# Optimization experiments

Hardware: AMD Instinct MI355X
Metric: run time of the kernel (lower is better)

Reference implementation:

```python
import jax, jax.numpy as jnp
import numpy as np

N = 262144
C = 81
NUM_HARD = 32768


def setup_inputs() -> dict:
    key = jax.random.key(0)
    k1, k2, k3, k4 = jax.random.split(key, 4)
    return {
        "cls_score": jax.random.normal(k1, (N, C), dtype=jnp.float32),
        "rois_label": jax.random.randint(k2, (N,), 0, C, dtype=jnp.int32),
        "bbox_pred": jax.random.normal(k3, (N, 4), dtype=jnp.float32),
        "rois_target": jax.random.normal(k4, (N, 4), dtype=jnp.float32),
        "rois_inside_ws": jnp.ones((N, 4), dtype=jnp.float32),
        "rois_outside_ws": jnp.ones((N, 4), dtype=jnp.float32),
        "num_hard": NUM_HARD,
    }


def reference(cls_score, rois_label, bbox_pred, rois_target,
              rois_inside_ws, rois_outside_ws, num_hard):
    num_classes = cls_score.shape[1]
    pos = rois_label > 0                                   # [N] bool
    num_pos = jnp.sum(pos.astype(jnp.float32))

    # --- hard-example mining on detached scores (no grad through selection) ---
    conf_p = jax.lax.stop_gradient(cls_score)              # [N, C]
    x_max = jnp.max(conf_p)                                # global scalar max (as in torch code)
    lse = jnp.log(jnp.sum(jnp.exp(conf_p - x_max), axis=1)) + x_max   # [N]
    gathered = jnp.take_along_axis(conf_p, rois_label[:, None].astype(jnp.int32), axis=1)[:, 0]
    loss_c = lse - gathered                                # [N]
    loss_c = jnp.where(pos, jnp.float32(100.0), loss_c)    # force positives in
    _, topk_idx = jax.lax.top_k(loss_c, num_hard)          # [num_hard]

    # --- weighted cross entropy on selected hard examples ---
    weight = jnp.ones((num_classes,), dtype=jnp.float32).at[0].set(num_pos / num_hard)
    sel_logits = cls_score[topk_idx]                       # [num_hard, C]
    sel_labels = rois_label[topk_idx]                      # [num_hard]
    logp = jax.nn.log_softmax(sel_logits, axis=1)
    nll = -jnp.take_along_axis(logp, sel_labels[:, None].astype(jnp.int32), axis=1)[:, 0]
    w = weight[sel_labels]
    loss_cls = jnp.sum(w * nll) / jnp.sum(w)               # torch weighted-mean CE

    # --- smooth L1 on positive rois only (masked; mean over num_pos*4 elems) ---
    diff = bbox_pred - rois_target                         # [N, 4]
    ad = jnp.abs(diff)
    sl1 = jnp.where(ad < 1.0, 0.5 * diff * diff, ad - 0.5)
    posf = pos.astype(sl1.dtype)[:, None]
    loss_box = jnp.sum(sl1 * posf) / (num_pos * 4.0)

    return loss_cls, loss_box
```

## Files before the change

kernel.cpp:

```cpp
#include <hip/hip_runtime.h>

#define NROWS 262144
#define NCLS  81
#define NTILES 4096
#define TILE_FLOATS 5184
#define KEY100 0xC2C80000u

__device__ __forceinline__ unsigned mono(float f) {
    unsigned u = __float_as_uint(f);
    return (u & 0x80000000u) ? ~u : (u | 0x80000000u);
}

__global__ __launch_bounds__(256) void row_kernel(
        const float* __restrict__ cls, const int* __restrict__ label,
        const float* __restrict__ bpred, const float* __restrict__ btgt,
        float4* __restrict__ partial)
{
    __shared__ float sm[TILE_FLOATS];
    __shared__ int slbl[64];
    __shared__ unsigned ru[3][4];
    __shared__ float rf[3][4];

    const int t = threadIdx.x;
    const int lane = t & 63, wid = t >> 6;
    const int blk = blockIdx.x;
    const int row = t >> 2, j = t & 3;

    int myLbl = label[blk*64 + row];
    if (t < 64) slbl[t] = label[blk*64 + t];
    float bsum = 0.f;
    {
        int gi = blk*256 + t;
        float p = bpred[gi], q = btgt[gi];
        if (myLbl > 0) {
            float d = p - q, ad = fabsf(d);
            bsum = (ad < 1.f) ? 0.5f*d*d : ad - 0.5f;
        }
    }

    {
        const float4* src = (const float4*)(cls + (size_t)blk * TILE_FLOATS);
        float4* dst = (float4*)sm;
        #pragma unroll
        for (int jj = 0; jj < 5; ++jj) dst[t + 256*jj] = src[t + 256*jj];
        if (t < 16) dst[t + 1280] = src[t + 1280];
    }
    __syncthreads();

    const float* rp = sm + row * NCLS;
    float s = 0.f;
    for (int i = j; i < NCLS; i += 4) s += __expf(rp[i]);
    s += __shfl_xor(s, 1);
    s += __shfl_xor(s, 2);

    unsigned pcnt = 0, gcnt = 0, ecnt = 0;
    float gtv = 0.f, pnv = 0.f;
    if (j == 0) {
        float lse = __logf(s);
        bool pos = myLbl > 0;
        float nll = lse - rp[myLbl];
        unsigned kk = mono(pos ? 100.0f : nll);
        pcnt = pos ? 1u : 0u;
        gcnt = (kk > KEY100) ? 1u : 0u;
        ecnt = (!pos && kk == KEY100) ? 1u : 0u;
        gtv  = (kk > KEY100) ? nll : 0.f;
        pnv  = pos ? nll : 0.f;
    }
    #pragma unroll
    for (int off = 32; off; off >>= 1) {
        pcnt += __shfl_xor(pcnt, off);
        gcnt += __shfl_xor(gcnt, off);
        ecnt += __shfl_xor(ecnt, off);
        gtv  += __shfl_xor(gtv, off);
        pnv  += __shfl_xor(pnv, off);
        bsum += __shfl_xor(bsum, off);
    }
    if (lane == 0) {
        ru[0][wid] = pcnt; ru[1][wid] = gcnt; ru[2][wid] = ecnt;
        rf[0][wid] = gtv;  rf[1][wid] = pnv;  rf[2][wid] = bsum;
    }
    __syncthreads();
    if (t == 0) {
        unsigned np = ru[0][0]+ru[0][1]+ru[0][2]+ru[0][3];
        unsigned ng = ru[1][0]+ru[1][1]+ru[1][2]+ru[1][3];
        unsigned ne = ru[2][0]+ru[2][1]+ru[2][2]+ru[2][3];
        float gt = rf[0][0]+rf[0][1]+rf[0][2]+rf[0][3];
        float pn = rf[1][0]+rf[1][1]+rf[1][2]+rf[1][3];
        float bx = rf[2][0]+rf[2][1]+rf[2][2]+rf[2][3];
        partial[blk] = make_float4(__uint_as_float(np | (ng<<8) | (ne<<16)), gt, pn, bx);
    }
}

__device__ void scan_desc_64k_1024(const unsigned* hist, unsigned k,
                                   unsigned* outB, unsigned* outRem,
                                   unsigned* wsum )
{
    const int t = threadIdx.x, lane = t & 63, wid = t >> 6;
    unsigned sum = 0;
    for (int j = 0; j < 64; ++j) sum += hist[65535 - (t*64 + j)];
    unsigned inc = sum;
    #pragma unroll
    for (int off = 1; off < 64; off <<= 1) {
        unsigned v = __shfl_up(inc, off);
        if (lane >= off) inc += v;
    }
    if (lane == 63) wsum[wid] = inc;
    __syncthreads();
    unsigned woff = 0;
    for (int w = 0; w < wid; ++w) woff += wsum[w];
    unsigned running = woff + inc - sum;
    for (int j = 0; j < 64; ++j) {
        unsigned bkt = 65535u - (unsigned)(t*64 + j);
        unsigned c = hist[bkt];
        if (running < k && running + c >= k) { *outB = bkt; *outRem = k - running; }
        running += c;
    }
}

__global__ __launch_bounds__(1024) void finalize_kernel(
        const float* __restrict__ cls, const int* __restrict__ label,
        const float4* __restrict__ partial, const int* __restrict__ d_num_hard,
        unsigned* __restrict__ hist, float* __restrict__ nllbuf,
        float* __restrict__ out)
{
    const int t = threadIdx.x, lane = t & 63, wid = t >> 6;
    __shared__ unsigned wNp[16], wNg[16], wNe[16];
    __shared__ float wPn[16], wGt[16], wBx[16];
    __shared__ unsigned sCross, sCumBefore;
    __shared__ float sFull, sPartial;
    __shared__ float sm[TILE_FLOATS];
    __shared__ float snll[64];
    __shared__ int slbl[64];

    unsigned npI[4]; float pnI[4];
    unsigned npS = 0, ngS = 0, neS = 0;
    float gtS = 0.f, pnS = 0.f, bxS = 0.f;
    #pragma unroll
    for (int i = 0; i < 4; ++i) {
        float4 v = partial[t*4 + i];
        unsigned c = __float_as_uint(v.x);
        npI[i] = c & 255u; pnI[i] = v.z;
        npS += npI[i]; ngS += (c >> 8) & 255u; neS += (c >> 16) & 255u;
        gtS += v.y; pnS += v.z; bxS += v.w;
    }
    unsigned incNp = npS; float incPn = pnS;
    #pragma unroll
    for (int off = 1; off < 64; off <<= 1) {
        unsigned v = __shfl_up(incNp, off);
        float    f = __shfl_up(incPn, off);
        if (lane >= off) { incNp += v; incPn += f; }
    }
    #pragma unroll
    for (int off = 32; off; off >>= 1) {
        ngS += __shfl_xor(ngS, off); neS += __shfl_xor(neS, off);
        gtS += __shfl_xor(gtS, off); bxS += __shfl_xor(bxS, off);
    }
    if (lane == 63) { wNp[wid] = incNp; wPn[wid] = incPn; }
    if (lane == 0)  { wNg[wid] = ngS; wNe[wid] = neS; wGt[wid] = gtS; wBx[wid] = bxS; }
    __syncthreads();

    unsigned NP = 0, NG = 0, NE = 0; float GT = 0.f, BX = 0.f;
    unsigned npOff = 0; float pnOff = 0.f;
    for (int w = 0; w < 16; ++w) {
        NP += wNp[w]; NG += wNg[w]; NE += wNe[w]; GT += wGt[w]; BX += wBx[w];
        if (w < wid) { npOff += wNp[w]; pnOff += wPn[w]; }
    }
    const unsigned k = (unsigned)(*d_num_hard);
    const bool fast = (NG < k) && (NG + NP >= k) && (NE == 0);

    if (fast) {
        const unsigned need = k - NG;
        unsigned cum = npOff + incNp - npS;
        float    fl  = pnOff + incPn - pnS;
        #pragma unroll
        for (int i = 0; i < 4; ++i) {
            if (cum < need && cum + npI[i] >= need) {
                sCross = (unsigned)(t*4 + i); sCumBefore = cum; sFull = fl;
            }
            cum += npI[i]; fl += pnI[i];
        }
        __syncthreads();

        {
            const float4* src = (const float4*)(cls + (size_t)sCross * TILE_FLOATS);
            float4* dst = (float4*)sm;
            dst[t] = src[t];
            if (t < 272) dst[t + 1024] = src[t + 1024];
            if (t < 64) slbl[t] = label[(int)sCross*64 + t];
        }
        __syncthreads();

        {
            const int brow = t >> 4, bj = t & 15;
            const float* rp = sm + brow * NCLS;
            float s = 0.f;
            for (int i = bj; i < NCLS; i += 16) s += __expf(rp[i]);
            s += __shfl_xor(s, 1);
            s += __shfl_xor(s, 2);
            s += __shfl_xor(s, 4);
            s += __shfl_xor(s, 8);
            if (bj == 0) snll[brow] = __logf(s) - rp[slbl[brow]];
        }
        __syncthreads();

        if (t < 64) {
            int lbl = slbl[t];
            bool pos = lbl > 0;
            unsigned long long m = __ballot(pos);
            unsigned rank = (unsigned)__popcll(m & ((1ull << t) - 1ull));
            unsigned rem = need - sCumBefore;
            float c = (pos && rank < rem) ? snll[t] : 0.f;
            #pragma unroll
            for (int off = 32; off; off >>= 1) c += __shfl_xor(c, off);
            if (t == 0) sPartial = c;
        }
        __syncthreads();
        if (t == 0) {
            float wgt0 = (float)NP / (float)k;
            out[0] = (wgt0*GT + sFull + sPartial) / (wgt0*NG + (float)need);
            out[1] = BX / ((float)NP * 4.0f);
        }
        return;
    }

    __shared__ unsigned wsum[16];
    __shared__ unsigned sB1, sKrem, sTkey, sNeed;
    __shared__ unsigned wEq[16];
    __shared__ float r1[16], r2[16];
    __syncthreads();

    for (int r = t; r < NROWS; r += 1024) {
        const float* rp = cls + (size_t)r * NCLS;
        float ssum = 0.f;
        for (int cix = 0; cix < NCLS; ++cix) ssum += __expf(rp[cix]);
        nllbuf[r] = __logf(ssum) - rp[label[r]];
    }
    __syncthreads();

    for (int i = t; i < 65536; i += 1024) hist[i] = 0u;
    __syncthreads();
    for (int base = 0; base < NROWS; base += 1024) {
        int r = base + t;
        unsigned key = mono(label[r] > 0 ? 100.0f : nllbuf[r]);
        unsigned bkt = key >> 16;
        unsigned long long active = __ballot(1);
        while (active) {
            int leader = (int)__builtin_ctzll(active);
            unsigned lb = __shfl(bkt, leader);
            unsigned long long grp = __ballot(bkt == lb) & active;
            if (lane == leader) atomicAdd(&hist[lb], (unsigned)__popcll(grp));
            active &= ~grp;
        }
    }
    __syncthreads();
    scan_desc_64k_1024(hist, k, &sB1, &sKrem, wsum);
    __syncthreads();

    for (int i = t; i < 65536; i += 1024) hist[i] = 0u;
    __syncthreads();
    for (int base = 0; base < NROWS; base += 1024) {
        int r = base + t;
        unsigned key = mono(label[r] > 0 ? 100.0f : nllbuf[r]);
        bool in = (key >> 16) == sB1;
        unsigned bkt = key & 0xFFFFu;
        unsigned long long active = __ballot(in);
        while (active) {
            int leader = (int)__builtin_ctzll(active);
            unsigned lb = __shfl(bkt, leader);
            unsigned long long grp = __ballot(in && bkt == lb) & active;
            if (lane == leader) atomicAdd(&hist[lb], (unsigned)__popcll(grp));
            active &= ~grp;
        }
    }
    __syncthreads();
    scan_desc_64k_1024(hist, sKrem, &sTkey, &sNeed, wsum);
    __syncthreads();
    if (t == 0) sTkey = (sB1 << 16) | sTkey;
    __syncthreads();

    const unsigned tkey = sTkey, need = sNeed;
    const float wgt0 = (float)NP / (float)k;
    float accN = 0.f, accW = 0.f;
    unsigned running = 0;
    for (int base = 0; base < NROWS; base += 1024) {
        int r = base + t;
        int lbl = label[r]; float v = nllbuf[r];
        unsigned key = mono(lbl > 0 ? 100.0f : v);
        bool eq = (key == tkey);
        unsigned long long b = __ballot(eq);
        if (lane == 0) wEq[wid] = (unsigned)__popcll(b);
        __syncthreads();
        unsigned woff = 0, chunkTotal = 0;
        for (int w = 0; w < 16; ++w) {
            chunkTotal += wEq[w];
            if (w < wid) woff += wEq[w];
        }
        unsigned rank = running + woff + (unsigned)__popcll(b & ((1ull << lane) - 1ull));
        bool sel = (key > tkey) || (eq && rank < need);
        if (sel) { float wg = (lbl == 0) ? wgt0 : 1.f; accN += wg * v; accW += wg; }
        running += chunkTotal;
        __syncthreads();
    }
    #pragma unroll
    for (int off = 32; off; off >>= 1) {
        accN += __shfl_xor(accN, off);
        accW += __shfl_xor(accW, off);
    }
    if (lane == 0) { r1[wid] = accN; r2[wid] = accW; }
    __syncthreads();
    if (t == 0) {
        float N = 0.f, W = 0.f;
        for (int w = 0; w < 16; ++w) { N += r1[w]; W += r2[w]; }
        out[0] = N / W;
        out[1] = BX / ((float)NP * 4.0f);
    }
}

extern "C" void kernel_launch(void* const* d_in, const int* in_sizes, int n_in,
                              void* d_out, int out_size, void* d_ws, size_t ws_size,
                              hipStream_t stream) {
    const float* cls   = (const float*)d_in[0];
    const int*   label = (const int*)d_in[1];
    const float* bpred = (const float*)d_in[2];
    const float* btgt  = (const float*)d_in[3];
    const int*   nh    = (const int*)d_in[6];
    float* out = (float*)d_out;

    char* ws = (char*)d_ws;
    float4*   partial = (float4*)(ws);
    unsigned* hist    = (unsigned*)(ws + 65536);
    float*    nllbuf  = (float*)(ws + 65536 + 262144);

    row_kernel<<<NTILES, 256, 0, stream>>>(cls, label, bpred, btgt, partial);
    finalize_kernel<<<1, 1024, 0, stream>>>(cls, label, partial, nh,
                                            hist, nllbuf, out);
}
```

Before: 29.15 us.

## Compute row exp-sums in registers with LDS atomics instead of staging tile

Stops staging the 64x81 logits tile in shared memory. Each thread now exponentiates its own coalesced float4 values in registers and accumulates per-row sums with shared-memory atomicAdd, splitting a float4 across rows where it straddles a row boundary. The per-row label logit is then read directly from global memory, and the count and partial-sum reductions are done by the first wave only. This is meant to cut LDS footprint, which could raise occupancy, and to remove a strided LDS read pass, at the cost of LDS atomic contention and an extra scattered global load per row.

```diff
diff --git a/kernel.cpp b/kernel.cpp
--- a/kernel.cpp
+++ b/kernel.cpp
@@ -16,18 +16,17 @@
         const float* __restrict__ bpred, const float* __restrict__ btgt,
         float4* __restrict__ partial)
 {
-    __shared__ float sm[TILE_FLOATS];
+    __shared__ float rowsum[64];
     __shared__ int slbl[64];
-    __shared__ unsigned ru[3][4];
-    __shared__ float rf[3][4];
+    __shared__ float wbs[4];
 
     const int t = threadIdx.x;
     const int lane = t & 63, wid = t >> 6;
     const int blk = blockIdx.x;
-    const int row = t >> 2, j = t & 3;
-
-    int myLbl = label[blk*64 + row];
-    if (t < 64) slbl[t] = label[blk*64 + t];
+
+    if (t < 64) { rowsum[t] = 0.f; slbl[t] = label[blk*64 + t]; }
+
+    int myLbl = label[blk*64 + (t >> 2)];
     float bsum = 0.f;
     {
         int gi = blk*256 + t;
@@ -38,56 +37,60 @@
         }
     }
 
-    {
-        const float4* src = (const float4*)(cls + (size_t)blk * TILE_FLOATS);
-        float4* dst = (float4*)sm;
+    const float4* src = (const float4*)(cls + (size_t)blk * TILE_FLOATS);
+    float4 v[6];
+    #pragma unroll
+    for (int jj = 0; jj < 6; ++jj)
+        if (jj < 5 || t < 16) v[jj] = src[t + 256*jj];
+
+    __syncthreads();
+
+    #pragma unroll
+    for (int jj = 0; jj < 6; ++jj) {
+        if (jj < 5 || t < 16) {
+            int le = (t + 256*jj) * 4;
+            int r0 = le / 81;
+            int c0 = le - r0*81;
+            float e0 = __expf(v[jj].x), e1 = __expf(v[jj].y);
+            float e2 = __expf(v[jj].z), e3 = __expf(v[jj].w);
+            if (c0 <= 77) {
+                atomicAdd(&rowsum[r0], (e0+e1)+(e2+e3));
+            } else {
+                int n0 = 81 - c0;
+                float a = e0 + (n0 > 1 ? e1 : 0.f) + (n0 > 2 ? e2 : 0.f);
+                float b = (n0 > 1 ? 0.f : e1) + (n0 > 2 ? 0.f : e2) + e3;
+                atomicAdd(&rowsum[r0], a);
+                atomicAdd(&rowsum[r0+1], b);
+            }
+        }
+    }
+    __syncthreads();
+
+    unsigned cnt = 0; float gtv = 0.f, pnv = 0.f;
+    if (t < 64) {
+        float lse = __logf(rowsum[t]);
+        int lbl = slbl[t];
+        bool pos = lbl > 0;
+        float nll = lse - cls[(size_t)(blk*64 + t)*NCLS + lbl];
+        unsigned kk = mono(pos ? 100.0f : nll);
+        cnt = (pos ? 1u : 0u) | ((kk > KEY100 ? 1u : 0u) << 8)
+            | (((!pos && kk == KEY100) ? 1u : 0u) << 16);
+        gtv = (kk > KEY100) ? nll : 0.f;
+        pnv = pos ? nll : 0.f;
         #pragma unroll
-        for (int jj = 0; jj < 5; ++jj) dst[t + 256*jj] = src[t + 256*jj];
-        if (t < 16) dst[t + 1280] = src[t + 1280];
-    }
-    __syncthreads();
-
-    const float* rp = sm + row * NCLS;
-    float s = 0.f;
-    for (int i = j; i < NCLS; i += 4) s += __expf(rp[i]);
-    s += __shfl_xor(s, 1);
-    s += __shfl_xor(s, 2);
-
-    unsigned pcnt = 0, gcnt = 0, ecnt = 0;
-    float gtv = 0.f, pnv = 0.f;
-    if (j == 0) {
-        float lse = __logf(s);
-        bool pos = myLbl > 0;
-        float nll = lse - rp[myLbl];
-        unsigned kk = mono(pos ? 100.0f : nll);
-        pcnt = pos ? 1u : 0u;
-        gcnt = (kk > KEY100) ? 1u : 0u;
-        ecnt = (!pos && kk == KEY100) ? 1u : 0u;
-        gtv  = (kk > KEY100) ? nll : 0.f;
-        pnv  = pos ? nll : 0.f;
-    }
-    #pragma unroll
-    for (int off = 32; off; off >>= 1) {
-        pcnt += __shfl_xor(pcnt, off);
-        gcnt += __shfl_xor(gcnt, off);
-        ecnt += __shfl_xor(ecnt, off);
-        gtv  += __shfl_xor(gtv, off);
-        pnv  += __shfl_xor(pnv, off);
-        bsum += __shfl_xor(bsum, off);
-    }
-    if (lane == 0) {
-        ru[0][wid] = pcnt; ru[1][wid] = gcnt; ru[2][wid] = ecnt;
-        rf[0][wid] = gtv;  rf[1][wid] = pnv;  rf[2][wid] = bsum;
-    }
+        for (int off = 32; off; off >>= 1) {
+            cnt += __shfl_xor(cnt, off);
+            gtv += __shfl_xor(gtv, off);
+            pnv += __shfl_xor(pnv, off);
+        }
+    }
+    #pragma unroll
+    for (int off = 32; off; off >>= 1) bsum += __shfl_xor(bsum, off);
+    if (lane == 0) wbs[wid] = bsum;
     __syncthreads();
     if (t == 0) {
-        unsigned np = ru[0][0]+ru[0][1]+ru[0][2]+ru[0][3];
-        unsigned ng = ru[1][0]+ru[1][1]+ru[1][2]+ru[1][3];
-        unsigned ne = ru[2][0]+ru[2][1]+ru[2][2]+ru[2][3];
-        float gt = rf[0][0]+rf[0][1]+rf[0][2]+rf[0][3];
-        float pn = rf[1][0]+rf[1][1]+rf[1][2]+rf[1][3];
-        float bx = rf[2][0]+rf[2][1]+rf[2][2]+rf[2][3];
-        partial[blk] = make_float4(__uint_as_float(np | (ng<<8) | (ne<<16)), gt, pn, bx);
+        float bx = wbs[0]+wbs[1]+wbs[2]+wbs[3];
+        partial[blk] = make_float4(__uint_as_float(cnt), gtv, pnv, bx);
     }
 }
 
```

Result: slower. 55.00 us (+88.6%).
